# Kernel optimization log

Measured on AMD Instinct MI355X. Metric: run time of the kernel, lower is better.

## Reference

```python
import jax, jax.numpy as jnp
import numpy as np

D, NH, NL, NP, DFF = 256, 8, 4, 4, 1024
HD = D // NH
SHAPES = np.array([[100, 152], [50, 76], [25, 38], [13, 19]], dtype=np.int64)
LV = int((SHAPES[:, 0] * SHAPES[:, 1]).sum())  # 20197


def setup_inputs() -> dict:
    key = jax.random.key(0)
    ks = iter(jax.random.split(key, 48))
    bs, Lq = 8, 300

    def w(shape, s=0.02):
        return jax.random.normal(next(ks), shape, jnp.float32) * s

    lsi = np.concatenate([[0], np.cumsum(SHAPES[:, 0] * SHAPES[:, 1])[:-1]]).astype(np.int64)
    return dict(
        tgt=w((bs, Lq, D), 1.0),
        query_pos=w((bs, Lq, D), 1.0),
        reference_points=jax.random.uniform(next(ks), (bs, Lq, NL, 2), jnp.float32),
        src=w((bs, LV, D), 1.0),
        in_proj_w=w((3 * D, D)), in_proj_b=jnp.zeros((3 * D,), jnp.float32),
        out_proj_w=w((D, D)), out_proj_b=jnp.zeros((D,), jnp.float32),
        samp_off_w=w((NH * NL * NP * 2, D)), samp_off_b=w((NH * NL * NP * 2,), 0.5),
        attn_w_w=w((NH * NL * NP, D)), attn_w_b=jnp.zeros((NH * NL * NP,), jnp.float32),
        value_proj_w=w((D, D)), value_proj_b=jnp.zeros((D,), jnp.float32),
        output_proj_w=w((D, D)), output_proj_b=jnp.zeros((D,), jnp.float32),
        lin1_w=w((DFF, D)), lin1_b=jnp.zeros((DFF,), jnp.float32),
        lin2_w=w((D, DFF)), lin2_b=jnp.zeros((D,), jnp.float32),
        norm1_w=jnp.ones((D,), jnp.float32), norm1_b=jnp.zeros((D,), jnp.float32),
        norm2_w=jnp.ones((D,), jnp.float32), norm2_b=jnp.zeros((D,), jnp.float32),
        norm3_w=jnp.ones((D,), jnp.float32), norm3_b=jnp.zeros((D,), jnp.float32),
        spatial_shapes=SHAPES,            # static numpy (shapes must be static)
        level_start_index=lsi,            # static numpy
        padding_mask=jnp.zeros((bs, LV), bool),
    )


def _ln(x, w, b):
    m = x.mean(-1, keepdims=True)
    v = ((x - m) ** 2).mean(-1, keepdims=True)
    return (x - m) * jax.lax.rsqrt(v + 1e-5) * w + b


def _bilinear(vflat, H_, W_, loc):
    # vflat: (b,h,H*W,d); loc: (b,h,q,p,2) normalized to [0,1]
    # matches F.grid_sample(align_corners=False, padding_mode='zeros')
    x = loc[..., 0] * W_ - 0.5
    y = loc[..., 1] * H_ - 0.5
    x0f, y0f = jnp.floor(x), jnp.floor(y)
    lx, ly = x - x0f, y - y0f
    x0, y0 = x0f.astype(jnp.int32), y0f.astype(jnp.int32)
    b, h, q, p = x0.shape

    def gather(ix, iy, wgt):
        valid = (ix >= 0) & (ix < W_) & (iy >= 0) & (iy < H_)
        idx = (jnp.clip(iy, 0, H_ - 1) * W_ + jnp.clip(ix, 0, W_ - 1)).reshape(b, h, q * p)
        g = jnp.take_along_axis(vflat, idx[..., None], axis=2)  # (b,h,q*p,d)
        return g * (wgt * valid).reshape(b, h, q * p, 1)

    out = (gather(x0, y0, (1 - lx) * (1 - ly)) + gather(x0 + 1, y0, lx * (1 - ly))
           + gather(x0, y0 + 1, (1 - lx) * ly) + gather(x0 + 1, y0 + 1, lx * ly))
    return out.reshape(b, h, q, p, -1)


def reference(tgt, query_pos, reference_points, src, in_proj_w, in_proj_b,
              out_proj_w, out_proj_b, samp_off_w, samp_off_b, attn_w_w, attn_w_b,
              value_proj_w, value_proj_b, output_proj_w, output_proj_b,
              lin1_w, lin1_b, lin2_w, lin2_b, norm1_w, norm1_b, norm2_w, norm2_b,
              norm3_w, norm3_b, spatial_shapes, level_start_index, padding_mask):
    bs, Lq, _ = tgt.shape
    ss = np.asarray(spatial_shapes)
    lsi = np.asarray(level_start_index)

    # ---- self attention (eval mode, dropout off) ----
    qk = tgt + query_pos
    qh = (qk @ in_proj_w[:D].T + in_proj_b[:D]).reshape(bs, Lq, NH, HD)
    kh = (qk @ in_proj_w[D:2 * D].T + in_proj_b[D:2 * D]).reshape(bs, Lq, NH, HD)
    vh = (tgt @ in_proj_w[2 * D:].T + in_proj_b[2 * D:]).reshape(bs, Lq, NH, HD)
    scores = jnp.einsum('bqhd,bkhd->bhqk', qh, kh) / jnp.sqrt(jnp.float32(HD))
    attn = jax.nn.softmax(scores, axis=-1)
    sa = jnp.einsum('bhqk,bkhd->bqhd', attn, vh).reshape(bs, Lq, D)
    sa = sa @ out_proj_w.T + out_proj_b
    x = _ln(tgt + sa, norm2_w, norm2_b)

    # ---- MSDeformAttn cross attention ----
    query = x + query_pos
    value = src @ value_proj_w.T + value_proj_b
    value = jnp.where(padding_mask[..., None], 0.0, value)
    value_t = value.reshape(bs, -1, NH, HD).transpose(0, 2, 1, 3)  # (b,h,Lv,d)

    offsets = (query @ samp_off_w.T + samp_off_b).reshape(bs, Lq, NH, NL, NP, 2)
    aw = jax.nn.softmax((query @ attn_w_w.T + attn_w_b).reshape(bs, Lq, NH, NL * NP), -1)
    aw = aw.reshape(bs, Lq, NH, NL, NP)
    norma = jnp.asarray(np.stack([ss[:, 1], ss[:, 0]], -1), jnp.float32)  # (NL,2)=[W,H]
    loc = reference_points[:, :, None, :, None, :] + offsets / norma[None, None, None, :, None, :]

    out = jnp.zeros((bs, Lq, NH, HD), value.dtype)
    for l in range(NL):
        H_, W_ = int(ss[l, 0]), int(ss[l, 1])
        s0 = int(lsi[l])
        vl = value_t[:, :, s0:s0 + H_ * W_]                    # (b,h,HW,d)
        ll = loc[:, :, :, l].transpose(0, 2, 1, 3, 4)          # (b,h,q,p,2)
        samp = _bilinear(vl, H_, W_, ll)                       # (b,h,q,p,d)
        out = out + jnp.einsum('bhqpd,bqhp->bqhd', samp, aw[:, :, :, l])
    ca = out.reshape(bs, Lq, D) @ output_proj_w.T + output_proj_b
    x = _ln(x + ca, norm1_w, norm1_b)

    # ---- FFN ----
    ffn = jax.nn.relu(x @ lin1_w.T + lin1_b) @ lin2_w.T + lin2_b
    x = _ln(x + ffn, norm3_w, norm3_b)
    return (x, loc, aw)
```

## Files before the change

kernel.cpp:

```cpp
#include <hip/hip_runtime.h>
#include <hip/hip_bf16.h>

#define D_ 256
#define NH_ 8
#define HD_ 32
#define NL_ 4
#define NP_ 4
#define DFF_ 1024
#define BS_ 8
#define LQ_ 300
#define LV_ 20197
#define NQ_ (BS_*LQ_)
#define NSRC_ (BS_*LV_*D_)

__device__ __forceinline__ float u2f(unsigned int u) {
    union { unsigned int i; float f; } v; v.i = u << 16; return v.f;
}
__device__ __forceinline__ float lo2f(unsigned int u) {
    union { unsigned int i; float f; } v; v.i = u << 16; return v.f;
}
__device__ __forceinline__ float hi2f(unsigned int u) {
    union { unsigned int i; float f; } v; v.i = u & 0xffff0000u; return v.f;
}
__device__ __forceinline__ unsigned short f2bf_bits(float f) {
    __hip_bfloat16 b = __float2bfloat16(f);
    union { __hip_bfloat16 b; unsigned short u; } v; v.b = b; return v.u;
}

#define DOT4(accum, wv, ap) do { \
    float4 _a = *(const float4*)(ap); \
    accum += wv.x*_a.x + wv.y*_a.y + wv.z*_a.z + wv.w*_a.w; } while(0)

__global__ __launch_bounds__(256) void cvt_bf16_kernel(
    const float* __restrict__ src, unsigned short* __restrict__ vbf)
{
    const int nsrc4 = NSRC_/4;
    for (int i = blockIdx.x*256 + threadIdx.x; i < nsrc4; i += gridDim.x*256) {
        float4 v = ((const float4*)src)[i];
        ushort4 o;
        o.x = f2bf_bits(v.x); o.y = f2bf_bits(v.y);
        o.z = f2bf_bits(v.z); o.w = f2bf_bits(v.w);
        ((ushort4*)vbf)[i] = o;
    }
}

__global__ __launch_bounds__(256) void pack_weights_kernel(
    const float4* __restrict__ ipw,  const float4* __restrict__ opw,
    const float4* __restrict__ sow,  const float4* __restrict__ aww,
    const float4* __restrict__ outw, const float4* __restrict__ l1w,
    const float4* __restrict__ l2w,  const float4* __restrict__ vpw,
    float4* __restrict__ ipwP,  float4* __restrict__ opwP,
    float4* __restrict__ sowP,  float4* __restrict__ awwP,
    float4* __restrict__ outwP, float4* __restrict__ l1wP,
    float4* __restrict__ l2wP,  float4* __restrict__ vpwP)
{
    __shared__ float4 tile[32][33];
    const int RS[8]  = {768,256,256,128,256,1024,256,256};
    const int C4S[8] = {64, 64, 64, 64, 64, 64, 256, 64};
    const int TCUM[9] = {0,48,64,80,88,104,168,232,248};
    int tb = blockIdx.x, mi = 0;
    while (tb >= TCUM[mi+1]) ++mi;
    const int lt = tb - TCUM[mi];
    const float4* in  = (mi==0)?ipw :(mi==1)?opw :(mi==2)?sow :(mi==3)?aww
                       :(mi==4)?outw:(mi==5)?l1w :(mi==6)?l2w :vpw;
    float4* out       = (mi==0)?ipwP:(mi==1)?opwP:(mi==2)?sowP:(mi==3)?awwP
                       :(mi==4)?outwP:(mi==5)?l1wP:(mi==6)?l2wP:vpwP;
    const int R = RS[mi], C4 = C4S[mi];
    const int tpr = C4 >> 5;
    const int by = lt / tpr, bx = lt % tpr;
    const int tx = threadIdx.x & 31, ty = threadIdx.x >> 5;
#pragma unroll
    for (int i = 0; i < 32; i += 8)
        tile[ty+i][tx] = in[(size_t)(by*32+ty+i)*C4 + bx*32+tx];
    __syncthreads();
#pragma unroll
    for (int i = 0; i < 32; i += 8)
        out[(size_t)(bx*32+ty+i)*R + by*32+tx] = tile[tx][ty+i];
}

__global__ __launch_bounds__(256) void qkv_kernel(
    const float* __restrict__ tgt, const float* __restrict__ qp,
    const float4* __restrict__ ipwP, const float* __restrict__ bias,
    float* __restrict__ qh, float* __restrict__ kh, float* __restrict__ vh)
{
    __shared__ float arow[8][D_];
    const int t = threadIdx.x, m0 = blockIdx.x * 8, pass = blockIdx.y;
    for (int r = 0; r < 8; ++r) {
        float tv = tgt[(m0+r)*D_ + t];
        arow[r][t] = (pass == 2) ? tv : tv + qp[(m0+r)*D_ + t];
    }
    __syncthreads();
    const float4* w4 = ipwP + pass*256 + t;
    float acc[8] = {0,0,0,0,0,0,0,0};
    for (int c = 0; c < 64; ++c) {
        float4 wv = w4[c*768];
#pragma unroll
        for (int r = 0; r < 8; ++r) DOT4(acc[r], wv, &arow[r][c*4]);
    }
    float bb = bias[pass*256 + t];
    float* dst = (pass == 0) ? qh : (pass == 1) ? kh : vh;
    for (int r = 0; r < 8; ++r) dst[(m0+r)*D_ + t] = acc[r] + bb;
}

__global__ __launch_bounds__(256) void attn_kernel(
    const float* __restrict__ qh, const float* __restrict__ kh,
    const float* __restrict__ vh, float* __restrict__ sa)
{
    __shared__ unsigned short khl[LQ_][HD_+2];
    __shared__ unsigned short vhl[LQ_][HD_+2];
    __shared__ float sc[4][LQ_];
    __shared__ float qbuf[4][HD_];
    const int b = blockIdx.x >> 3, h = blockIdx.x & 7, chunk = blockIdx.y;
    const int t = threadIdx.x, w = t >> 6, lane = t & 63;
    for (int i = t; i < LQ_*HD_; i += 256) {
        int kq = i >> 5, d = i & 31;
        khl[kq][d] = f2bf_bits(kh[(b*LQ_ + kq)*D_ + h*HD_ + d]);
        vhl[kq][d] = f2bf_bits(vh[(b*LQ_ + kq)*D_ + h*HD_ + d]);
    }
    __syncthreads();
    const float scale = 0.17677669529663687f;
    for (int qi = 0; qi < 15; ++qi) {
        const int q = chunk*60 + w*15 + qi;
        if (lane < HD_) qbuf[w][lane] = qh[(b*LQ_ + q)*D_ + h*HD_ + lane];
        float qv[HD_];
#pragma unroll
        for (int d2 = 0; d2 < HD_; ++d2) qv[d2] = qbuf[w][d2];
        float mx = -1e30f;
        for (int k = lane; k < LQ_; k += 64) {
            float s = 0.f;
#pragma unroll
            for (int d2 = 0; d2 < HD_; ++d2) s += qv[d2]*u2f(khl[k][d2]);
            s *= scale;
            sc[w][k] = s;
            mx = fmaxf(mx, s);
        }
#pragma unroll
        for (int off = 32; off; off >>= 1) mx = fmaxf(mx, __shfl_xor(mx, off));
        float lsum = 0.f;
        for (int k = lane; k < LQ_; k += 64) {
            float e = __expf(sc[w][k] - mx);
            sc[w][k] = e; lsum += e;
        }
#pragma unroll
        for (int off = 32; off; off >>= 1) lsum += __shfl_xor(lsum, off);
        const int d = lane & 31, half = lane >> 5;
        float acc = 0.f;
        for (int k = half*150; k < half*150 + 150; ++k) acc += sc[w][k]*u2f(vhl[k][d]);
        acc += __shfl_down(acc, 32);
        if (lane < 32) sa[(b*LQ_ + q)*D_ + h*HD_ + d] = acc / lsum;
    }
}

__global__ __launch_bounds__(256) void proj_res_ln_kernel(
    const float* __restrict__ A, const float4* __restrict__ WP,
    const float* __restrict__ bias, const float* __restrict__ res,
    const float* __restrict__ gw, const float* __restrict__ gb,
    float* __restrict__ out)
{
    __shared__ float arow[8][D_];
    __shared__ float2 part[4][8];
    const int t = threadIdx.x, m0 = blockIdx.x * 8;
    const int w = t >> 6, lane = t & 63;
    for (int r = 0; r < 8; ++r) arow[r][t] = A[(m0+r)*D_ + t];
    __syncthreads();
    float acc[8] = {0,0,0,0,0,0,0,0};
    const float4* w4 = WP + t;
    for (int c = 0; c < 64; ++c) {
        float4 wv = w4[c*256];
#pragma unroll
        for (int r = 0; r < 8; ++r) DOT4(acc[r], wv, &arow[r][c*4]);
    }
    const float bb = bias[t], gwv = gw[t], gbv = gb[t];
    float v[8];
#pragma unroll
    for (int r = 0; r < 8; ++r) {
        v[r] = acc[r] + bb + res[(m0+r)*D_+t];
        float s = v[r], ss = v[r]*v[r];
#pragma unroll
        for (int off = 32; off; off >>= 1) {
            s += __shfl_xor(s, off); ss += __shfl_xor(ss, off);
        }
        if (lane == 0) part[w][r] = make_float2(s, ss);
    }
    __syncthreads();
#pragma unroll
    for (int r = 0; r < 8; ++r) {
        float2 p0 = part[0][r], p1 = part[1][r], p2 = part[2][r], p3 = part[3][r];
        float mean = (p0.x+p1.x+p2.x+p3.x) * (1.0f/256.0f);
        float ex2  = (p0.y+p1.y+p2.y+p3.y) * (1.0f/256.0f);
        float var  = ex2 - mean*mean;
        out[(m0+r)*D_+t] = (v[r]-mean) * rsqrtf(var + 1e-5f) * gwv + gbv;
    }
}

__global__ __launch_bounds__(256) void samp_params_kernel(
    const float* __restrict__ x1, const float* __restrict__ qp,
    const float4* __restrict__ sowP, const float* __restrict__ so_b,
    const float4* __restrict__ awwP, const float* __restrict__ aw_b,
    const float* __restrict__ refp,
    float* __restrict__ loc_out, float* __restrict__ aw_out)
{
    __shared__ float qrow[8][D_];
    __shared__ float logits[8][128];
    const int t = threadIdx.x, m0 = blockIdx.x * 8;
    for (int r = 0; r < 8; ++r)
        qrow[r][t] = x1[(m0+r)*D_ + t] + qp[(m0+r)*D_ + t];
    __syncthreads();
    {
        float acc[8] = {0,0,0,0,0,0,0,0};
        const float4* w4 = sowP + t;
        for (int c = 0; c < 64; ++c) {
            float4 wv = w4[c*256];
#pragma unroll
            for (int r = 0; r < 8; ++r) DOT4(acc[r], wv, &qrow[r][c*4]);
        }
        const float ob = so_b[t];
        const int c_ = t & 1, l_ = (t >> 3) & 3;
        float nrm;
        if (c_ == 0) nrm = (l_==0)?152.f:(l_==1)?76.f:(l_==2)?38.f:19.f;
        else         nrm = (l_==0)?100.f:(l_==1)?50.f:(l_==2)?25.f:13.f;
        for (int r = 0; r < 8; ++r) {
            int m = m0 + r;
            float off = acc[r] + ob;
            loc_out[m*256 + t] = refp[(m*NL_ + l_)*2 + c_] + off / nrm;
        }
    }
    if (t < 128) {
        float acc[8] = {0,0,0,0,0,0,0,0};
        const float4* w4 = awwP + t;
        for (int c = 0; c < 64; ++c) {
            float4 wv = w4[c*128];
#pragma unroll
            for (int r = 0; r < 8; ++r) DOT4(acc[r], wv, &qrow[r][c*4]);
        }
        const float ab = aw_b[t];
        for (int r = 0; r < 8; ++r) logits[r][t] = acc[r] + ab;
    }
    __syncthreads();
    if (t < 128) {
        const int g0 = (t >> 4) << 4;
        for (int r = 0; r < 8; ++r) {
            float mx = -1e30f;
            for (int j = 0; j < 16; ++j) mx = fmaxf(mx, logits[r][g0+j]);
            float s = 0.f;
            for (int j = 0; j < 16; ++j) s += __expf(logits[r][g0+j] - mx);
            aw_out[(m0+r)*128 + t] = __expf(logits[r][t] - mx) / s;
        }
    }
}

__global__ __launch_bounds__(256) void samp_fuse_bf16_kernel(
    const unsigned short* __restrict__ vbf,
    const float* __restrict__ loc_f, const float* __restrict__ aw_f,
    float* __restrict__ svec_g, float* __restrict__ wsum_g)
{
    __shared__ int   cidx[128][4];
    __shared__ float cwt[128][4];
    const int m = blockIdx.x, t = threadIdx.x;
    const int b = m / LQ_;

    if (t < 128) {
        const int l = (t >> 2) & 3;
        const int HS[4] = {100,50,25,13}, WS[4] = {152,76,38,19}, S0[4] = {0,15200,19000,19950};
        const int Hh = HS[l], Ww = WS[l], s0 = S0[l];
        const float aw = aw_f[m*128 + t];
        const float x = loc_f[m*256 + 2*t]*Ww - 0.5f;
        const float y = loc_f[m*256 + 2*t + 1]*Hh - 0.5f;
        const float x0f = floorf(x), y0f = floorf(y);
        const int x0 = (int)x0f, y0 = (int)y0f;
        const float fx = x - x0f, fy = y - y0f;
        const int   cx[4] = {x0, x0+1, x0,   x0+1};
        const int   cy[4] = {y0, y0,   y0+1, y0+1};
        const float cw[4] = {(1.f-fx)*(1.f-fy), fx*(1.f-fy), (1.f-fx)*fy, fx*fy};
        float sw = 0.f;
#pragma unroll
        for (int j = 0; j < 4; ++j) {
            const bool valid = (cx[j] >= 0) & (cx[j] < Ww) & (cy[j] >= 0) & (cy[j] < Hh);
            cidx[t][j] = valid ? (s0 + cy[j]*Ww + cx[j]) : s0;
            float wv = valid ? aw*cw[j] : 0.f;
            cwt[t][j] = wv;
            sw += wv;
        }
#pragma unroll
        for (int off = 8; off; off >>= 1) sw += __shfl_xor(sw, off);
        if ((t & 15) == 0) wsum_g[m*NH_ + (t >> 4)] = sw;
    }
    __syncthreads();

    const int hh = (t >> 7) * 4;
    const int c  = t & 127;
    const unsigned int* sb = (const unsigned int*)(vbf + (size_t)b*LV_*D_) + c;
#pragma unroll
    for (int h = hh; h < hh + 4; ++h) {
        float e0=0.f, e1=0.f, e2=0.f, e3=0.f;
        float o0=0.f, o1=0.f, o2=0.f, o3=0.f;
#pragma unroll 4
        for (int s = 0; s < 16; ++s) {
            const int base = h*16 + s;
            const int   i0 = cidx[base][0], i1 = cidx[base][1],
                        i2 = cidx[base][2], i3 = cidx[base][3];
            const float w0 = cwt[base][0], w1 = cwt[base][1],
                        w2 = cwt[base][2], w3 = cwt[base][3];
            const unsigned int u0 = sb[(size_t)i0*128];
            const unsigned int u1 = sb[(size_t)i1*128];
            const unsigned int u2 = sb[(size_t)i2*128];
            const unsigned int u3 = sb[(size_t)i3*128];
            e0 += w0*lo2f(u0); o0 += w0*hi2f(u0);
            e1 += w1*lo2f(u1); o1 += w1*hi2f(u1);
            e2 += w2*lo2f(u2); o2 += w2*hi2f(u2);
            e3 += w3*lo2f(u3); o3 += w3*hi2f(u3);
        }
        *(float2*)&svec_g[(size_t)m*(NH_*D_) + h*D_ + 2*c] =
            make_float2((e0+e1)+(e2+e3), (o0+o1)+(o2+o3));
    }
}

__global__ __launch_bounds__(256) void vproj_kernel(
    const float* __restrict__ svec_g, const float* __restrict__ wsum_g,
    const float4* __restrict__ vpwP, const float* __restrict__ vpb,
    float* __restrict__ vo)
{
    __shared__ float sv[4][NH_*D_];
    const int t = threadIdx.x, m0 = blockIdx.x * 4;
    for (int i = t; i < 4*NH_*D_; i += 256)
        sv[i >> 11][i & 2047] = svec_g[(size_t)m0*(NH_*D_) + i];
    __syncthreads();
    const int h = t >> 5;
    const float4* w4 = vpwP + t;
    float a0 = 0.f, a1 = 0.f, a2 = 0.f, a3 = 0.f;
    for (int c = 0; c < 64; ++c) {
        const float4 wq = w4[c*256];
        const float4 s0 = *(const float4*)&sv[0][h*D_ + c*4];
        const float4 s1 = *(const float4*)&sv[1][h*D_ + c*4];
        const float4 s2 = *(const float4*)&sv[2][h*D_ + c*4];
        const float4 s3 = *(const float4*)&sv[3][h*D_ + c*4];
        a0 += wq.x*s0.x + wq.y*s0.y + wq.z*s0.z + wq.w*s0.w;
        a1 += wq.x*s1.x + wq.y*s1.y + wq.z*s1.z + wq.w*s1.w;
        a2 += wq.x*s2.x + wq.y*s2.y + wq.z*s2.z + wq.w*s2.w;
        a3 += wq.x*s3.x + wq.y*s3.y + wq.z*s3.z + wq.w*s3.w;
    }
    const float bb = vpb[t];
    vo[(size_t)(m0+0)*D_ + t] = a0 + bb*wsum_g[(m0+0)*NH_ + h];
    vo[(size_t)(m0+1)*D_ + t] = a1 + bb*wsum_g[(m0+1)*NH_ + h];
    vo[(size_t)(m0+2)*D_ + t] = a2 + bb*wsum_g[(m0+2)*NH_ + h];
    vo[(size_t)(m0+3)*D_ + t] = a3 + bb*wsum_g[(m0+3)*NH_ + h];
}

__global__ __launch_bounds__(256) void samp_fuse_f32_kernel(
    const float* __restrict__ src, const float* __restrict__ Wv,
    const float* __restrict__ vpb,
    const float* __restrict__ loc_f, const float* __restrict__ aw_f,
    float* __restrict__ vo)
{
    __shared__ float svec[NH_][D_];
    __shared__ int   cidx[128][4];
    __shared__ float cwt[128][4];
    __shared__ float wsum[NH_];
    const int m = blockIdx.x, t = threadIdx.x;
    const int b = m / LQ_;

    if (t < 128) {
        const int l = (t >> 2) & 3;
        const int HS[4] = {100,50,25,13}, WS[4] = {152,76,38,19}, S0[4] = {0,15200,19000,19950};
        const int Hh = HS[l], Ww = WS[l], s0 = S0[l];
        const float aw = aw_f[m*128 + t];
        const float x = loc_f[m*256 + 2*t]*Ww - 0.5f;
        const float y = loc_f[m*256 + 2*t + 1]*Hh - 0.5f;
        const float x0f = floorf(x), y0f = floorf(y);
        const int x0 = (int)x0f, y0 = (int)y0f;
        const float fx = x - x0f, fy = y - y0f;
        const int   cx[4] = {x0, x0+1, x0,   x0+1};
        const int   cy[4] = {y0, y0,   y0+1, y0+1};
        const float cw[4] = {(1.f-fx)*(1.f-fy), fx*(1.f-fy), (1.f-fx)*fy, fx*fy};
        float sw = 0.f;
#pragma unroll
        for (int jj = 0; jj < 4; ++jj) {
            const bool valid = (cx[jj] >= 0) & (cx[jj] < Ww) & (cy[jj] >= 0) & (cy[jj] < Hh);
            cidx[t][jj] = valid ? (s0 + cy[jj]*Ww + cx[jj]) : s0;
            float wv = valid ? aw*cw[jj] : 0.f;
            cwt[t][jj] = wv;
            sw += wv;
        }
#pragma unroll
        for (int off = 8; off; off >>= 1) sw += __shfl_xor(sw, off);
        if ((t & 15) == 0) wsum[t >> 4] = sw;
    }
    __syncthreads();

    const float* sb = src + (size_t)b*LV_*D_ + t;
#pragma unroll
    for (int h = 0; h < NH_; ++h) {
        float a0 = 0.f, a1 = 0.f, a2 = 0.f, a3 = 0.f;
#pragma unroll 4
        for (int s = 0; s < 16; ++s) {
            const int base = h*16 + s;
            const int   i0 = cidx[base][0], i1 = cidx[base][1],
                        i2 = cidx[base][2], i3 = cidx[base][3];
            const float w0 = cwt[base][0], w1 = cwt[base][1],
                        w2 = cwt[base][2], w3 = cwt[base][3];
            a0 += w0 * sb[(size_t)i0*D_];
            a1 += w1 * sb[(size_t)i1*D_];
            a2 += w2 * sb[(size_t)i2*D_];
            a3 += w3 * sb[(size_t)i3*D_];
        }
        svec[h][t] = (a0 + a1) + (a2 + a3);
    }
    __syncthreads();

    const int h = t >> 5;
    const float4* w4 = (const float4*)(Wv + t*D_);
    float a = 0.f;
    for (int c = 0; c < 64; ++c) {
        float4 wv = w4[c];
        DOT4(a, wv, &svec[h][c*4]);
    }
    vo[m*D_ + t] = a + vpb[t]*wsum[h];
}

__global__ __launch_bounds__(256) void ffn1_kernel(
    const float* __restrict__ x2, const float4* __restrict__ l1wP,
    const float* __restrict__ b1, float* __restrict__ hid)
{
    __shared__ float arow[8][D_];
    const int t = threadIdx.x, m0 = blockIdx.x * 8, cc = blockIdx.y;
    for (int r = 0; r < 8; ++r) arow[r][t] = x2[(m0+r)*D_ + t];
    __syncthreads();
    const int j = cc*256 + t;
    float acc[8] = {0,0,0,0,0,0,0,0};
    const float4* w4 = l1wP + j;
    for (int c = 0; c < 64; ++c) {
        float4 wv = w4[c*1024];
#pragma unroll
        for (int r = 0; r < 8; ++r) DOT4(acc[r], wv, &arow[r][c*4]);
    }
    const float bb = b1[j];
    for (int r = 0; r < 8; ++r) {
        float v = acc[r] + bb;
        hid[(m0+r)*DFF_ + j] = v > 0.f ? v : 0.f;
    }
}

__global__ __launch_bounds__(256) void ffn2_ln_kernel(
    const float* __restrict__ hid, const float4* __restrict__ l2wP,
    const float* __restrict__ b2, const float* __restrict__ res,
    const float* __restrict__ gw, const float* __restrict__ gb,
    float* __restrict__ out)
{
    __shared__ float hrow[8][DFF_];
    __shared__ float2 part[4][8];
    const int t = threadIdx.x, m0 = blockIdx.x * 8;
    const int w = t >> 6, lane = t & 63;
    for (int i = t; i < 8*DFF_; i += 256)
        hrow[i >> 10][i & 1023] = hid[(m0 + (i >> 10))*DFF_ + (i & 1023)];
    __syncthreads();
    float acc[8] = {0,0,0,0,0,0,0,0};
    const float4* w4 = l2wP + t;
    for (int c = 0; c < 256; ++c) {
        float4 wv = w4[c*256];
#pragma unroll
        for (int r = 0; r < 8; ++r) DOT4(acc[r], wv, &hrow[r][c*4]);
    }
    const float bb = b2[t], gwv = gw[t], gbv = gb[t];
    float v[8];
#pragma unroll
    for (int r = 0; r < 8; ++r) {
        v[r] = acc[r] + bb + res[(m0+r)*D_+t];
        float s = v[r], ss = v[r]*v[r];
#pragma unroll
        for (int off = 32; off; off >>= 1) {
            s += __shfl_xor(s, off); ss += __shfl_xor(ss, off);
        }
        if (lane == 0) part[w][r] = make_float2(s, ss);
    }
    __syncthreads();
#pragma unroll
    for (int r = 0; r < 8; ++r) {
        float2 p0 = part[0][r], p1 = part[1][r], p2 = part[2][r], p3 = part[3][r];
        float mean = (p0.x+p1.x+p2.x+p3.x) * (1.0f/256.0f);
        float ex2  = (p0.y+p1.y+p2.y+p3.y) * (1.0f/256.0f);
        float var  = ex2 - mean*mean;
        out[(m0+r)*D_+t] = (v[r]-mean) * rsqrtf(var + 1e-5f) * gwv + gbv;
    }
}

extern "C" void kernel_launch(void* const* d_in, const int* in_sizes, int n_in,
                              void* d_out, int out_size, void* d_ws, size_t ws_size,
                              hipStream_t stream) {
    (void)in_sizes; (void)n_in; (void)out_size;
    const float* tgt  = (const float*)d_in[0];
    const float* qpos = (const float*)d_in[1];
    const float* refp = (const float*)d_in[2];
    const float* srcp = (const float*)d_in[3];
    const float* ipw  = (const float*)d_in[4];
    const float* ipb  = (const float*)d_in[5];
    const float* opw  = (const float*)d_in[6];
    const float* opb  = (const float*)d_in[7];
    const float* sow  = (const float*)d_in[8];
    const float* sob  = (const float*)d_in[9];
    const float* aww  = (const float*)d_in[10];
    const float* awb  = (const float*)d_in[11];
    const float* vpw  = (const float*)d_in[12];
    const float* vpb  = (const float*)d_in[13];
    const float* outw = (const float*)d_in[14];
    const float* outb = (const float*)d_in[15];
    const float* l1w  = (const float*)d_in[16];
    const float* l1b  = (const float*)d_in[17];
    const float* l2w  = (const float*)d_in[18];
    const float* l2b  = (const float*)d_in[19];
    const float* n1w  = (const float*)d_in[20];
    const float* n1b  = (const float*)d_in[21];
    const float* n2w  = (const float*)d_in[22];
    const float* n2b  = (const float*)d_in[23];
    const float* n3w  = (const float*)d_in[24];
    const float* n3b  = (const float*)d_in[25];

    float* wsf = (float*)d_ws;
    float* qh   = wsf;
    float* kh   = wsf + 614400;
    float* vh   = wsf + 1228800;
    float* sa   = wsf + 1843200;
    float* x1   = wsf + 2457600;
    float* vo   = wsf + 3072000;
    float* x2   = wsf + 3686400;
    float* hid  = wsf + 4300800;
    float* P0    = wsf + 6758400;
    float4* ipwP  = (float4*)(P0);
    float4* opwP  = (float4*)(P0 + 196608);
    float4* sowP  = (float4*)(P0 + 262144);
    float4* awwP  = (float4*)(P0 + 327680);
    float4* outwP = (float4*)(P0 + 360448);
    float4* l1wP  = (float4*)(P0 + 425984);
    float4* l2wP  = (float4*)(P0 + 688128);
    float4* vpwP  = (float4*)(P0 + 950272);
    unsigned short* vbf = (unsigned short*)(wsf + 7774208);
    float* svec_g = wsf + 7774208 + 20681728;
    float* wsum_g = svec_g + 4915200;
    const size_t need_bytes = (size_t)(7774208 + 20681728 + 4915200 + 19200) * 4;
    const bool use_bf16 = ws_size >= need_bytes;

    float* xout   = (float*)d_out;
    float* locout = xout + 614400;
    float* awout  = xout + 1228800;

    pack_weights_kernel<<<248, 256, 0, stream>>>(
        (const float4*)ipw, (const float4*)opw, (const float4*)sow,
        (const float4*)aww, (const float4*)outw, (const float4*)l1w,
        (const float4*)l2w, (const float4*)vpw,
        ipwP, opwP, sowP, awwP, outwP, l1wP, l2wP, vpwP);
    if (use_bf16)
        cvt_bf16_kernel<<<2048, 256, 0, stream>>>(srcp, vbf);
    qkv_kernel<<<dim3(NQ_/8, 3), 256, 0, stream>>>(tgt, qpos, ipwP, ipb, qh, kh, vh);
    attn_kernel<<<dim3(BS_*NH_, 5), 256, 0, stream>>>(qh, kh, vh, sa);
    proj_res_ln_kernel<<<NQ_/8, 256, 0, stream>>>(sa, opwP, opb, tgt, n2w, n2b, x1);
    samp_params_kernel<<<NQ_/8, 256, 0, stream>>>(x1, qpos, sowP, sob, awwP, awb, refp,
                                                  locout, awout);
    if (use_bf16) {
        samp_fuse_bf16_kernel<<<NQ_, 256, 0, stream>>>(vbf, locout, awout, svec_g, wsum_g);
        vproj_kernel<<<NQ_/4, 256, 0, stream>>>(svec_g, wsum_g, vpwP, vpb, vo);
    } else {
        samp_fuse_f32_kernel<<<NQ_, 256, 0, stream>>>(srcp, vpw, vpb, locout, awout, vo);
    }
    proj_res_ln_kernel<<<NQ_/8, 256, 0, stream>>>(vo, outwP, outb, x1, n1w, n1b, x2);
    ffn1_kernel<<<dim3(NQ_/8, 4), 256, 0, stream>>>(x2, l1wP, l1b, hid);
    ffn2_ln_kernel<<<NQ_/8, 256, 0, stream>>>(hid, l2wP, l2b, x2, n3w, n3b, xout);
}
```

Before: 673.7 us.

## Read GEMM activation rows directly from global memory instead of LDS staging

All the small GEMM kernels (qkv, projections, sampling params, FFN) stop staging their 8 activation rows in shared memory and instead read float4s straight from global memory, with unroll-by-4 on the reduction loop. The query+pos additions are precomputed: a new add_qk kernel produces tgt+query_pos once, and the first projection/LN kernel also emits x1+query_pos. This removes the LDS copy and barrier and the redundant adds, but relies on uniform broadcast loads hitting cache and adds an extra kernel launch plus extra workspace.

```diff
diff --git a/kernel.cpp b/kernel.cpp
--- a/kernel.cpp
+++ b/kernel.cpp
@@ -42,6 +42,15 @@
         o.z = f2bf_bits(v.z); o.w = f2bf_bits(v.w);
         ((ushort4*)vbf)[i] = o;
     }
+}
+
+__global__ __launch_bounds__(256) void add_qk_kernel(
+    const float* __restrict__ tgt, const float* __restrict__ qp,
+    float* __restrict__ qk)
+{
+    const int i = blockIdx.x*256 + threadIdx.x;
+    float4 a = ((const float4*)tgt)[i], b = ((const float4*)qp)[i];
+    ((float4*)qk)[i] = make_float4(a.x+b.x, a.y+b.y, a.z+b.z, a.w+b.w);
 }
 
 __global__ __launch_bounds__(256) void pack_weights_kernel(
@@ -79,23 +88,19 @@
 }
 
 __global__ __launch_bounds__(256) void qkv_kernel(
-    const float* __restrict__ tgt, const float* __restrict__ qp,
+    const float* __restrict__ qk, const float* __restrict__ tgt,
     const float4* __restrict__ ipwP, const float* __restrict__ bias,
     float* __restrict__ qh, float* __restrict__ kh, float* __restrict__ vh)
 {
-    __shared__ float arow[8][D_];
     const int t = threadIdx.x, m0 = blockIdx.x * 8, pass = blockIdx.y;
-    for (int r = 0; r < 8; ++r) {
-        float tv = tgt[(m0+r)*D_ + t];
-        arow[r][t] = (pass == 2) ? tv : tv + qp[(m0+r)*D_ + t];
-    }
-    __syncthreads();
+    const float* a0 = ((pass == 2) ? tgt : qk) + (size_t)m0*D_;
     const float4* w4 = ipwP + pass*256 + t;
     float acc[8] = {0,0,0,0,0,0,0,0};
+#pragma unroll 4
     for (int c = 0; c < 64; ++c) {
         float4 wv = w4[c*768];
 #pragma unroll
-        for (int r = 0; r < 8; ++r) DOT4(acc[r], wv, &arow[r][c*4]);
+        for (int r = 0; r < 8; ++r) DOT4(acc[r], wv, a0 + r*D_ + c*4);
     }
     float bb = bias[pass*256 + t];
     float* dst = (pass == 0) ? qh : (pass == 1) ? kh : vh;
@@ -155,20 +160,20 @@
     const float* __restrict__ A, const float4* __restrict__ WP,
     const float* __restrict__ bias, const float* __restrict__ res,
     const float* __restrict__ gw, const float* __restrict__ gb,
-    float* __restrict__ out)
-{
-    __shared__ float arow[8][D_];
+    float* __restrict__ out, const float* __restrict__ qp,
+    float* __restrict__ outq)
+{
     __shared__ float2 part[4][8];
     const int t = threadIdx.x, m0 = blockIdx.x * 8;
     const int w = t >> 6, lane = t & 63;
-    for (int r = 0; r < 8; ++r) arow[r][t] = A[(m0+r)*D_ + t];
-    __syncthreads();
+    const float* a0 = A + (size_t)m0*D_;
     float acc[8] = {0,0,0,0,0,0,0,0};
     const float4* w4 = WP + t;
+#pragma unroll 4
     for (int c = 0; c < 64; ++c) {
         float4 wv = w4[c*256];
 #pragma unroll
-        for (int r = 0; r < 8; ++r) DOT4(acc[r], wv, &arow[r][c*4]);
+        for (int r = 0; r < 8; ++r) DOT4(acc[r], wv, a0 + r*D_ + c*4);
     }
     const float bb = bias[t], gwv = gw[t], gbv = gb[t];
     float v[8];
@@ -189,30 +194,30 @@
         float mean = (p0.x+p1.x+p2.x+p3.x) * (1.0f/256.0f);
         float ex2  = (p0.y+p1.y+p2.y+p3.y) * (1.0f/256.0f);
         float var  = ex2 - mean*mean;
-        out[(m0+r)*D_+t] = (v[r]-mean) * rsqrtf(var + 1e-5f) * gwv + gbv;
+        float o = (v[r]-mean) * rsqrtf(var + 1e-5f) * gwv + gbv;
+        out[(m0+r)*D_+t] = o;
+        if (outq) outq[(m0+r)*D_+t] = o + qp[(m0+r)*D_+t];
     }
 }
 
 __global__ __launch_bounds__(256) void samp_params_kernel(
-    const float* __restrict__ x1, const float* __restrict__ qp,
+    const float* __restrict__ x1q,
     const float4* __restrict__ sowP, const float* __restrict__ so_b,
     const float4* __restrict__ awwP, const float* __restrict__ aw_b,
     const float* __restrict__ refp,
     float* __restrict__ loc_out, float* __restrict__ aw_out)
 {
-    __shared__ float qrow[8][D_];
     __shared__ float logits[8][128];
     const int t = threadIdx.x, m0 = blockIdx.x * 8;
-    for (int r = 0; r < 8; ++r)
-        qrow[r][t] = x1[(m0+r)*D_ + t] + qp[(m0+r)*D_ + t];
-    __syncthreads();
+    const float* a0 = x1q + (size_t)m0*D_;
     {
         float acc[8] = {0,0,0,0,0,0,0,0};
         const float4* w4 = sowP + t;
+#pragma unroll 4
         for (int c = 0; c < 64; ++c) {
             float4 wv = w4[c*256];
 #pragma unroll
-            for (int r = 0; r < 8; ++r) DOT4(acc[r], wv, &qrow[r][c*4]);
+            for (int r = 0; r < 8; ++r) DOT4(acc[r], wv, a0 + r*D_ + c*4);
         }
         const float ob = so_b[t];
         const int c_ = t & 1, l_ = (t >> 3) & 3;
@@ -228,10 +233,11 @@
     if (t < 128) {
         float acc[8] = {0,0,0,0,0,0,0,0};
         const float4* w4 = awwP + t;
+#pragma unroll 4
         for (int c = 0; c < 64; ++c) {
             float4 wv = w4[c*128];
 #pragma unroll
-            for (int r = 0; r < 8; ++r) DOT4(acc[r], wv, &qrow[r][c*4]);
+            for (int r = 0; r < 8; ++r) DOT4(acc[r], wv, a0 + r*D_ + c*4);
         }
         const float ab = aw_b[t];
         for (int r = 0; r < 8; ++r) logits[r][t] = acc[r] + ab;
@@ -421,17 +427,16 @@
     const float* __restrict__ x2, const float4* __restrict__ l1wP,
     const float* __restrict__ b1, float* __restrict__ hid)
 {
-    __shared__ float arow[8][D_];
     const int t = threadIdx.x, m0 = blockIdx.x * 8, cc = blockIdx.y;
-    for (int r = 0; r < 8; ++r) arow[r][t] = x2[(m0+r)*D_ + t];
-    __syncthreads();
+    const float* a0 = x2 + (size_t)m0*D_;
     const int j = cc*256 + t;
     float acc[8] = {0,0,0,0,0,0,0,0};
     const float4* w4 = l1wP + j;
+#pragma unroll 4
     for (int c = 0; c < 64; ++c) {
         float4 wv = w4[c*1024];
 #pragma unroll
-        for (int r = 0; r < 8; ++r) DOT4(acc[r], wv, &arow[r][c*4]);
+        for (int r = 0; r < 8; ++r) DOT4(acc[r], wv, a0 + r*D_ + c*4);
     }
     const float bb = b1[j];
     for (int r = 0; r < 8; ++r) {
@@ -446,19 +451,17 @@
     const float* __restrict__ gw, const float* __restrict__ gb,
     float* __restrict__ out)
 {
-    __shared__ float hrow[8][DFF_];
     __shared__ float2 part[4][8];
     const int t = threadIdx.x, m0 = blockIdx.x * 8;
     const int w = t >> 6, lane = t & 63;
-    for (int i = t; i < 8*DFF_; i += 256)
-        hrow[i >> 10][i & 1023] = hid[(m0 + (i >> 10))*DFF_ + (i & 1023)];
-    __syncthreads();
+    const float* h0 = hid + (size_t)m0*DFF_;
     float acc[8] = {0,0,0,0,0,0,0,0};
     const float4* w4 = l2wP + t;
+#pragma unroll 4
     for (int c = 0; c < 256; ++c) {
         float4 wv = w4[c*256];
 #pragma unroll
-        for (int r = 0; r < 8; ++r) DOT4(acc[r], wv, &hrow[r][c*4]);
+        for (int r = 0; r < 8; ++r) DOT4(acc[r], wv, h0 + r*DFF_ + c*4);
     }
     const float bb = b2[t], gwv = gw[t], gbv = gb[t];
     float v[8];
@@ -523,7 +526,9 @@
     float* vo   = wsf + 3072000;
     float* x2   = wsf + 3686400;
     float* hid  = wsf + 4300800;
-    float* P0    = wsf + 6758400;
+    float* qk   = wsf + 6758400;
+    float* x1q  = wsf + 7372800;
+    float* P0   = wsf + 7987200;
     float4* ipwP  = (float4*)(P0);
     float4* opwP  = (float4*)(P0 + 196608);
     float4* sowP  = (float4*)(P0 + 262144);
@@ -532,10 +537,10 @@
     float4* l1wP  = (float4*)(P0 + 425984);
     float4* l2wP  = (float4*)(P0 + 688128);
     float4* vpwP  = (float4*)(P0 + 950272);
-    unsigned short* vbf = (unsigned short*)(wsf + 7774208);
-    float* svec_g = wsf + 7774208 + 20681728;
+    unsigned short* vbf = (unsigned short*)(wsf + 9003008);
+    float* svec_g = wsf + 9003008 + 20681728;
     float* wsum_g = svec_g + 4915200;
-    const size_t need_bytes = (size_t)(7774208 + 20681728 + 4915200 + 19200) * 4;
+    const size_t need_bytes = (size_t)(9003008 + 20681728 + 4915200 + 19200) * 4;
     const bool use_bf16 = ws_size >= need_bytes;
 
     float* xout   = (float*)d_out;
@@ -547,12 +552,14 @@
         (const float4*)aww, (const float4*)outw, (const float4*)l1w,
         (const float4*)l2w, (const float4*)vpw,
         ipwP, opwP, sowP, awwP, outwP, l1wP, l2wP, vpwP);
+    add_qk_kernel<<<600, 256, 0, stream>>>(tgt, qpos, qk);
     if (use_bf16)
         cvt_bf16_kernel<<<2048, 256, 0, stream>>>(srcp, vbf);
-    qkv_kernel<<<dim3(NQ_/8, 3), 256, 0, stream>>>(tgt, qpos, ipwP, ipb, qh, kh, vh);
+    qkv_kernel<<<dim3(NQ_/8, 3), 256, 0, stream>>>(qk, tgt, ipwP, ipb, qh, kh, vh);
     attn_kernel<<<dim3(BS_*NH_, 5), 256, 0, stream>>>(qh, kh, vh, sa);
-    proj_res_ln_kernel<<<NQ_/8, 256, 0, stream>>>(sa, opwP, opb, tgt, n2w, n2b, x1);
-    samp_params_kernel<<<NQ_/8, 256, 0, stream>>>(x1, qpos, sowP, sob, awwP, awb, refp,
+    proj_res_ln_kernel<<<NQ_/8, 256, 0, stream>>>(sa, opwP, opb, tgt, n2w, n2b,
+                                                  x1, qpos, x1q);
+    samp_params_kernel<<<NQ_/8, 256, 0, stream>>>(x1q, sowP, sob, awwP, awb, refp,
                                                   locout, awout);
     if (use_bf16) {
         samp_fuse_bf16_kernel<<<NQ_, 256, 0, stream>>>(vbf, locout, awout, svec_g, wsum_g);
@@ -560,7 +567,8 @@
     } else {
         samp_fuse_f32_kernel<<<NQ_, 256, 0, stream>>>(srcp, vpw, vpb, locout, awout, vo);
     }
-    proj_res_ln_kernel<<<NQ_/8, 256, 0, stream>>>(vo, outwP, outb, x1, n1w, n1b, x2);
+    proj_res_ln_kernel<<<NQ_/8, 256, 0, stream>>>(vo, outwP, outb, x1, n1w, n1b,
+                                                  x2, nullptr, nullptr);
     ffn1_kernel<<<dim3(NQ_/8, 4), 256, 0, stream>>>(x2, l1wP, l1b, hid);
     ffn2_ln_kernel<<<NQ_/8, 256, 0, stream>>>(hid, l2wP, l2b, x2, n3w, n3b, xout);
 }
```

Measured after the change: 656.4 us. 2.6% less time.
